# Kernel optimization log

Hardware: AMD Instinct MI355X
Metric: run time of the kernel (lower is better)

Reference implementation:

```python
import jax, jax.numpy as jnp
import numpy as np
from jax import lax

N = 25600      # total nodes = G * T
E = 204800     # edges (before self loops)
IN_CH = 6
HID = 64
HEADS = 4
G = 512        # graphs per batch
T = 50         # sequence length (node_time in [0, T))
OUT = 30       # prediction_horizon * 3
NEG_SLOPE = 0.2
BN_EPS = 1e-5


def _gat(x, src, dst, W, a_src, a_dst, b, heads, outc):
    # PyG GATConv (concat=True): h = x W reshaped to (N, H, C)
    n = x.shape[0]
    h = (x @ W).reshape(n, heads, outc)
    # edge scores: leaky_relu(a_src . h_src + a_dst . h_dst), softmax over incoming edges of dst
    e = jax.nn.leaky_relu((h * a_src).sum(-1)[src] + (h * a_dst).sum(-1)[dst], NEG_SLOPE)  # (E, H)
    m = jax.ops.segment_max(e, dst, num_segments=n)
    ex = jnp.exp(e - m[dst])
    denom = jax.ops.segment_sum(ex, dst, num_segments=n)
    alpha = ex / denom[dst]
    out = jax.ops.segment_sum(alpha[:, :, None] * h[src], dst, num_segments=n)  # (N, H, C)
    return out.reshape(n, heads * outc) + b


def _bn_eval(x, g, b):
    # BatchNorm in eval with running_mean=0, running_var=1
    return g * (x * (1.0 / np.float32(np.sqrt(1.0 + BN_EPS)))) + b


def setup_inputs() -> dict:
    ks = jax.random.split(jax.random.key(0), 16)
    s = 0.1
    d = {}
    d["x"] = jax.random.normal(ks[0], (N, IN_CH), jnp.float32)
    d["edge_index"] = jax.random.randint(ks[1], (2, E), 0, N)
    idx = jnp.arange(N)
    d["batch"] = idx // T       # each graph has exactly T nodes
    d["node_time"] = idx % T
    d["W1"] = jax.random.normal(ks[2], (IN_CH, HEADS * HID), jnp.float32) * s
    d["att_src1"] = jax.random.normal(ks[3], (HEADS, HID), jnp.float32) * s
    d["att_dst1"] = jax.random.normal(ks[4], (HEADS, HID), jnp.float32) * s
    d["b1"] = jnp.zeros((HEADS * HID,), jnp.float32)
    d["g1"] = jnp.ones((HEADS * HID,), jnp.float32)
    d["be1"] = jnp.zeros((HEADS * HID,), jnp.float32)
    d["W2"] = jax.random.normal(ks[5], (HEADS * HID, HID), jnp.float32) * s
    d["att_src2"] = jax.random.normal(ks[6], (1, HID), jnp.float32) * s
    d["att_dst2"] = jax.random.normal(ks[7], (1, HID), jnp.float32) * s
    d["b2"] = jnp.zeros((HID,), jnp.float32)
    d["g2"] = jnp.ones((HID,), jnp.float32)
    d["be2"] = jnp.zeros((HID,), jnp.float32)
    d["Wih"] = jax.random.normal(ks[8], (4 * HID, HID), jnp.float32) * s
    d["Whh"] = jax.random.normal(ks[9], (4 * HID, HID), jnp.float32) * s
    d["bih"] = jnp.zeros((4 * HID,), jnp.float32)
    d["bhh"] = jnp.zeros((4 * HID,), jnp.float32)
    d["Wfc"] = jax.random.normal(ks[10], (HID, OUT), jnp.float32) * s
    d["bfc"] = jnp.zeros((OUT,), jnp.float32)
    return d


def reference(x, edge_index, batch, node_time, W1, att_src1, att_dst1, b1, g1, be1,
              W2, att_src2, att_dst2, b2, g2, be2, Wih, Whh, bih, bhh, Wfc, bfc):
    loops = jnp.arange(N)
    src = jnp.concatenate([edge_index[0], loops])  # GATConv adds self loops
    dst = jnp.concatenate([edge_index[1], loops])
    h = jax.nn.elu(_bn_eval(_gat(x, src, dst, W1, att_src1, att_dst1, b1, HEADS, HID), g1, be1))
    h = jax.nn.elu(_bn_eval(_gat(h, src, dst, W2, att_src2, att_dst2, b2, 1, HID), g2, be2))
    # vectorized replacement of the per-node python scatter loop
    x_seq = jnp.zeros((G, T, HID), h.dtype).at[batch, node_time].set(h)

    def step(carry, xt):
        hh, cc = carry
        gates = xt @ Wih.T + bih + hh @ Whh.T + bhh
        i, f, gg, o = jnp.split(gates, 4, axis=-1)
        cc = jax.nn.sigmoid(f) * cc + jax.nn.sigmoid(i) * jnp.tanh(gg)
        hh = jax.nn.sigmoid(o) * jnp.tanh(cc)
        return (hh, cc), None

    init = (jnp.zeros((G, HID), h.dtype), jnp.zeros((G, HID), h.dtype))
    (hn, _), _ = lax.scan(step, init, x_seq.transpose(1, 0, 2))  # scan over time
    return hn @ Wfc + bfc  # (G, 30)
```

## Files before the change

### kernel.cpp

```cpp
#include <hip/hip_runtime.h>

#define N_NODES 25600
#define N_EDGES 204800
#define EE (N_EDGES + N_NODES)
#define IN_CH 6
#define HID 64
#define HEADS 4
#define G_GRAPHS 512
#define T_STEPS 50
#define OUT_DIM 30
#define NEG_SLOPE 0.2f
#define BN_INV 0.9999950000374997f

__device__ __forceinline__ float lrelu_(float x){ return x > 0.f ? x : NEG_SLOPE * x; }
__device__ __forceinline__ float elu_(float x){ return x > 0.f ? x : __expf(x) - 1.f; }
__device__ __forceinline__ float sigmoid_(float x){
    return __builtin_amdgcn_rcpf(1.f + __expf(-x));
}
__device__ __forceinline__ float tanh_(float x){
    return 1.f - 2.f * __builtin_amdgcn_rcpf(1.f + __expf(2.f * x));
}
__device__ __forceinline__ float bcast_(float v, int l){
    return __int_as_float(__builtin_amdgcn_readlane(__float_as_int(v), l));
}

__global__ void count_k(const int* __restrict__ ei, int* __restrict__ counts){
    int e = blockIdx.x * 256 + threadIdx.x;
    if (e >= EE) return;
    int dst = (e < N_EDGES) ? ei[N_EDGES + e] : (e - N_EDGES);
    atomicAdd(&counts[dst], 1);
}

__global__ void scan_k(const int* __restrict__ counts, int* __restrict__ row_ptr,
                       int* __restrict__ cursor){
    __shared__ int part[1024];
    int t = threadIdx.x;
    const int CH = N_NODES / 1024;
    int base = t * CH;
    int s = 0;
    for (int i = 0; i < CH; i++) s += counts[base + i];
    part[t] = s;
    __syncthreads();
    for (int off = 1; off < 1024; off <<= 1){
        int v = (t >= off) ? part[t - off] : 0;
        __syncthreads();
        part[t] += v;
        __syncthreads();
    }
    int run = (t > 0) ? part[t - 1] : 0;
    for (int i = 0; i < CH; i++){
        int cv = counts[base + i];
        row_ptr[base + i] = run;
        cursor[base + i]  = run;
        run += cv;
    }
    if (t == 1023) row_ptr[N_NODES] = run;
}

__global__ void scatter_k(const int* __restrict__ ei, int* __restrict__ cursor,
                          int* __restrict__ ssrc){
    int e = blockIdx.x * 256 + threadIdx.x;
    if (e >= EE) return;
    int src, dst;
    if (e < N_EDGES){ src = ei[e]; dst = ei[N_EDGES + e]; }
    else            { src = dst = e - N_EDGES; }
    int pos = atomicAdd(&cursor[dst], 1);
    ssrc[pos] = src;
}

__global__ void twih_k(const float* __restrict__ Wih, float* __restrict__ WihT){
    __shared__ float tile[64][65];
    int t = threadIdx.x;
    int jb = blockIdx.x * 64;
    for (int i = t; i < 64 * 64; i += 256){
        int j = i >> 6, k = i & 63;
        tile[k][j] = Wih[(size_t)(jb + j) * 64 + k];
    }
    __syncthreads();
    for (int i = t; i < 64 * 64; i += 256){
        int k = i >> 6, j = i & 63;
        WihT[(size_t)k * 256 + jb + j] = tile[k][j];
    }
}

__global__ void ns_k(const float* __restrict__ x, const float* __restrict__ W1,
                     const float* __restrict__ asw, const float* __restrict__ adw,
                     float* __restrict__ as1, float* __restrict__ ad1){
    __shared__ float waS[IN_CH * 4], waD[IN_CH * 4];
    int t = threadIdx.x;
    if (t < 48){
        int k = t >> 3, h = (t >> 1) & 3, which = t & 1;
        const float* a = which ? adw : asw;
        float s = 0.f;
        #pragma unroll
        for (int c = 0; c < 64; c++) s += W1[k * 256 + h * 64 + c] * a[h * 64 + c];
        (which ? waD : waS)[k * 4 + h] = s;
    }
    __syncthreads();
    int n = blockIdx.x * 256 + t;
    float xv[IN_CH];
    #pragma unroll
    for (int k = 0; k < IN_CH; k++) xv[k] = x[n * IN_CH + k];
    float sv[4] = {0.f, 0.f, 0.f, 0.f}, dv[4] = {0.f, 0.f, 0.f, 0.f};
    #pragma unroll
    for (int k = 0; k < IN_CH; k++){
        #pragma unroll
        for (int h = 0; h < 4; h++){
            sv[h] += xv[k] * waS[k * 4 + h];
            dv[h] += xv[k] * waD[k * 4 + h];
        }
    }
    *(float4*)&as1[n * 4] = make_float4(sv[0], sv[1], sv[2], sv[3]);
    *(float4*)&ad1[n * 4] = make_float4(dv[0], dv[1], dv[2], dv[3]);
}

__global__ void gat1_aggx(const float* __restrict__ x, const float* __restrict__ as1,
                          const float* __restrict__ ad1, const int* __restrict__ row_ptr,
                          const int* __restrict__ ssrc, const float* __restrict__ W1,
                          const float* __restrict__ b1, const float* __restrict__ g1,
                          const float* __restrict__ be1, float* __restrict__ h1_act){
    __shared__ float w1s[IN_CH * 256];
    int tid = threadIdx.x;
    for (int i = tid; i < IN_CH * 256; i += 256) w1s[i] = W1[i];
    __syncthreads();
    int wv = tid >> 6, lane = tid & 63;
    int n = blockIdx.x * 4 + wv;
    int s0 = row_ptr[n], s1 = row_ptr[n + 1];
    float4 adn = *(const float4*)&ad1[n * 4];
    float xs0[IN_CH] = {}, xs1[IN_CH] = {}, xs2[IN_CH] = {}, xs3[IN_CH] = {};
    float d0 = 0.f, d1 = 0.f, d2 = 0.f, d3 = 0.f;
    for (int j = s0; j < s1; j++){
        int s = ssrc[j];
        float4 as = *(const float4*)&as1[s * 4];
        float e0 = __expf(lrelu_(as.x + adn.x));
        float e1 = __expf(lrelu_(as.y + adn.y));
        float e2 = __expf(lrelu_(as.z + adn.z));
        float e3 = __expf(lrelu_(as.w + adn.w));
        d0 += e0; d1 += e1; d2 += e2; d3 += e3;
        const float2* xp = (const float2*)(x + (size_t)s * IN_CH);
        float2 xa = xp[0], xb = xp[1], xc = xp[2];
        float xv[IN_CH] = {xa.x, xa.y, xb.x, xb.y, xc.x, xc.y};
        #pragma unroll
        for (int k = 0; k < IN_CH; k++){
            xs0[k] += e0 * xv[k];
            xs1[k] += e1 * xv[k];
            xs2[k] += e2 * xv[k];
            xs3[k] += e3 * xv[k];
        }
    }
    float r0 = 1.f / d0, r1 = 1.f / d1, r2 = 1.f / d2, r3 = 1.f / d3;
    #pragma unroll
    for (int h = 0; h < 4; h++){
        const float* xsh = (h == 0) ? xs0 : (h == 1) ? xs1 : (h == 2) ? xs2 : xs3;
        float rh = (h == 0) ? r0 : (h == 1) ? r1 : (h == 2) ? r2 : r3;
        int col = h * 64 + lane;
        float acc = 0.f;
        #pragma unroll
        for (int k = 0; k < IN_CH; k++) acc += xsh[k] * w1s[k * 256 + col];
        float v = acc * rh + b1[col];
        v = g1[col] * (v * BN_INV) + be1[col];
        h1_act[(size_t)n * 256 + col] = elu_(v);
    }
}

#define TM 64
#define KT 32
#define APAD 4
__global__ __launch_bounds__(256) void gat2_tr(const float* __restrict__ h1_act,
                        const float* __restrict__ W2,
                        const float* __restrict__ asw, const float* __restrict__ adw,
                        float* __restrict__ h2_pre, float* __restrict__ as2,
                        float* __restrict__ ad2){
    __shared__ float As[TM][KT + APAD];
    __shared__ float Bs[KT][64];
    int tx = threadIdx.x;
    int rg = tx >> 4;
    int cg = tx & 15;
    int r0 = rg * 4, c0 = cg * 4;
    int rowBase = blockIdx.x * TM;
    float acc[4][4] = {};
    for (int k0 = 0; k0 < 256; k0 += KT){
        #pragma unroll
        for (int it = 0; it < 2; it++){
            int i = tx + it * 256;
            int row = i >> 3;
            int c4  = (i & 7) * 4;
            *(float4*)&As[row][c4] =
                *(const float4*)(h1_act + (size_t)(rowBase + row) * 256 + k0 + c4);
        }
        #pragma unroll
        for (int it = 0; it < 2; it++){
            int i = tx + it * 256;
            int row = i >> 4;
            int c4  = (i & 15) * 4;
            *(float4*)&Bs[row][c4] = *(const float4*)(W2 + (size_t)(k0 + row) * 64 + c4);
        }
        __syncthreads();
        #pragma unroll
        for (int kq = 0; kq < KT; kq += 4){
            float4 b0 = *(float4*)&Bs[kq + 0][c0];
            float4 b1v = *(float4*)&Bs[kq + 1][c0];
            float4 b2v = *(float4*)&Bs[kq + 2][c0];
            float4 b3 = *(float4*)&Bs[kq + 3][c0];
            #pragma unroll
            for (int i = 0; i < 4; i++){
                float4 a = *(float4*)&As[r0 + i][kq];
                acc[i][0] += a.x * b0.x + a.y * b1v.x + a.z * b2v.x + a.w * b3.x;
                acc[i][1] += a.x * b0.y + a.y * b1v.y + a.z * b2v.y + a.w * b3.y;
                acc[i][2] += a.x * b0.z + a.y * b1v.z + a.z * b2v.z + a.w * b3.z;
                acc[i][3] += a.x * b0.w + a.y * b1v.w + a.z * b2v.w + a.w * b3.w;
            }
        }
        __syncthreads();
    }
    float aw0 = asw[c0], aw1 = asw[c0+1], aw2 = asw[c0+2], aw3 = asw[c0+3];
    float dw0 = adw[c0], dw1 = adw[c0+1], dw2 = adw[c0+2], dw3 = adw[c0+3];
    #pragma unroll
    for (int i = 0; i < 4; i++){
        int row = rowBase + r0 + i;
        *(float4*)(h2_pre + (size_t)row * 64 + c0) =
            make_float4(acc[i][0], acc[i][1], acc[i][2], acc[i][3]);
        float sA = acc[i][0]*aw0 + acc[i][1]*aw1 + acc[i][2]*aw2 + acc[i][3]*aw3;
        float sD = acc[i][0]*dw0 + acc[i][1]*dw1 + acc[i][2]*dw2 + acc[i][3]*dw3;
        #pragma unroll
        for (int off = 8; off; off >>= 1){
            sA += __shfl_xor(sA, off);
            sD += __shfl_xor(sD, off);
        }
        if (cg == 0){ as2[row] = sA; ad2[row] = sD; }
    }
}

__global__ __launch_bounds__(256, 2) void gat2_aggp(const float* __restrict__ h2_pre,
        const float* __restrict__ as2, const float* __restrict__ ad2,
        const int* __restrict__ row_ptr, const int* __restrict__ ssrc,
        const float* __restrict__ b2, const float* __restrict__ g2,
        const float* __restrict__ be2,
        const int* __restrict__ batch, const int* __restrict__ ntime,
        const float* __restrict__ WihT, const float* __restrict__ bih,
        const float* __restrict__ bhh, float* __restrict__ gx){
    __shared__ float vsh[16][64];
    __shared__ int posb[16];
    int tx = threadIdx.x, wv = tx >> 6, lane = tx & 63;
    int nbase = blockIdx.x * 16;
    for (int q = 0; q < 4; q++){
        int n = nbase + wv * 4 + q;
        int s0 = row_ptr[n], s1 = row_ptr[n + 1];
        float adn = ad2[n];
        float denom = 0.f, acc = 0.f;
        int j = s0;
        for (; j + 4 <= s1; j += 4){
            int sa = ssrc[j], sb = ssrc[j + 1], sc = ssrc[j + 2], sd = ssrc[j + 3];
            float ea = __expf(lrelu_(as2[sa] + adn));
            float eb = __expf(lrelu_(as2[sb] + adn));
            float ec = __expf(lrelu_(as2[sc] + adn));
            float ed = __expf(lrelu_(as2[sd] + adn));
            float ha = h2_pre[(size_t)sa * 64 + lane];
            float hb = h2_pre[(size_t)sb * 64 + lane];
            float hc = h2_pre[(size_t)sc * 64 + lane];
            float hd = h2_pre[(size_t)sd * 64 + lane];
            denom += (ea + eb) + (ec + ed);
            acc += ea * ha + eb * hb + ec * hc + ed * hd;
        }
        for (; j < s1; j++){
            int s = ssrc[j];
            float e = __expf(lrelu_(as2[s] + adn));
            denom += e;
            acc += e * h2_pre[(size_t)s * 64 + lane];
        }
        float v = acc / denom + b2[lane];
        v = g2[lane] * (v * BN_INV) + be2[lane];
        vsh[wv * 4 + q][lane] = elu_(v);
        if (lane == 0) posb[wv * 4 + q] = batch[n] * T_STEPS + ntime[n];
    }
    __syncthreads();
    float vq[16];
    #pragma unroll
    for (int q = 0; q < 16; q++) vq[q] = vsh[q][lane];
    float bsum = bih[tx] + bhh[tx];
    float acc[16];
    #pragma unroll
    for (int q = 0; q < 16; q++) acc[q] = bsum;
    #pragma unroll 4
    for (int k = 0; k < 64; k++){
        float wk = WihT[(size_t)k * 256 + tx];
        #pragma unroll
        for (int q = 0; q < 16; q++)
            acc[q] += wk * bcast_(vq[q], k);
    }
    #pragma unroll
    for (int q = 0; q < 16; q++)
        gx[(size_t)posb[q] * 256 + tx] = acc[q];
}

__global__ __launch_bounds__(512, 2) void lstm_k(const float* __restrict__ gx,
        const float* __restrict__ Whh,
        const float* __restrict__ Wfc, const float* __restrict__ bfc,
        float* __restrict__ out){
    int g0 = blockIdx.x * 2;
    int t0 = threadIdx.x;
    int gr = t0 >> 8;
    int j  = t0 & 255;
    int lane = t0 & 63;
    __shared__ float gates[2][2][256];
    const float4* Wr = (const float4*)(Whh + (size_t)j * 64);
    const float* gxg = gx + (size_t)(g0 + gr) * T_STEPS * 256 + j;
    float c = 0.f, hn = 0.f;
    for (int t = 0; t < T_STEPS; t++){
        int buf = t & 1;
        float a0 = gxg[t * 256], a1 = 0.f, a2 = 0.f, a3 = 0.f;
        #pragma unroll
        for (int k = 0; k < 16; k++){
            float4 wv = Wr[k];
            a0 += wv.x * bcast_(hn, 4 * k + 0);
            a1 += wv.y * bcast_(hn, 4 * k + 1);
            a2 += wv.z * bcast_(hn, 4 * k + 2);
            a3 += wv.w * bcast_(hn, 4 * k + 3);
        }
        gates[gr][buf][j] = (a0 + a1) + (a2 + a3);
        __syncthreads();
        float iv = gates[gr][buf][lane];
        float fv = gates[gr][buf][64 + lane];
        float gv = gates[gr][buf][128 + lane];
        float ov = gates[gr][buf][192 + lane];
        c = sigmoid_(fv) * c + sigmoid_(iv) * tanh_(gv);
        hn = sigmoid_(ov) * tanh_(c);
    }
    if (j < 64) gates[gr][0][j] = hn;
    __syncthreads();
    if (j < OUT_DIM){
        float acc = bfc[j];
        #pragma unroll
        for (int k = 0; k < 64; k++) acc += gates[gr][0][k] * Wfc[k * OUT_DIM + j];
        out[(g0 + gr) * OUT_DIM + j] = acc;
    }
}

extern "C" void kernel_launch(void* const* d_in, const int* in_sizes, int n_in,
                              void* d_out, int out_size, void* d_ws, size_t ws_size,
                              hipStream_t stream){
    const float* x    = (const float*)d_in[0];
    const int*   ei   = (const int*)  d_in[1];
    const int*   batch= (const int*)  d_in[2];
    const int*   ntime= (const int*)  d_in[3];
    const float* W1   = (const float*)d_in[4];
    const float* as1w = (const float*)d_in[5];
    const float* ad1w = (const float*)d_in[6];
    const float* b1   = (const float*)d_in[7];
    const float* g1   = (const float*)d_in[8];
    const float* be1  = (const float*)d_in[9];
    const float* W2   = (const float*)d_in[10];
    const float* as2w = (const float*)d_in[11];
    const float* ad2w = (const float*)d_in[12];
    const float* b2   = (const float*)d_in[13];
    const float* g2   = (const float*)d_in[14];
    const float* be2  = (const float*)d_in[15];
    const float* Wih  = (const float*)d_in[16];
    const float* Whh  = (const float*)d_in[17];
    const float* bih  = (const float*)d_in[18];
    const float* bhh  = (const float*)d_in[19];
    const float* Wfc  = (const float*)d_in[20];
    const float* bfc  = (const float*)d_in[21];
    float* out = (float*)d_out;

    char* w = (char*)d_ws;
    auto alloc = [&](size_t bytes)->char*{
        char* p = w;
        w += (bytes + 255) & ~size_t(255);
        return p;
    };
    float* h1_act = (float*)alloc((size_t)N_NODES * 256 * 4);
    float* gx     = (float*)alloc((size_t)N_NODES * 256 * 4);
    float* h2_pre = (float*)alloc((size_t)N_NODES * 64 * 4);
    float* WihT   = (float*)alloc((size_t)64 * 256 * 4);
    float* as1    = (float*)alloc((size_t)N_NODES * 4 * 4);
    float* ad1    = (float*)alloc((size_t)N_NODES * 4 * 4);
    float* as2    = (float*)alloc((size_t)N_NODES * 4);
    float* ad2    = (float*)alloc((size_t)N_NODES * 4);
    int* counts   = (int*)alloc((size_t)N_NODES * 4);
    int* row_ptr  = (int*)alloc((size_t)(N_NODES + 1) * 4);
    int* cursor   = (int*)alloc((size_t)N_NODES * 4);
    int* ssrc     = (int*)alloc((size_t)EE * 4);

    hipMemsetAsync(counts, 0, (size_t)N_NODES * 4, stream);
    count_k  <<<(EE + 255) / 256, 256, 0, stream>>>(ei, counts);
    scan_k   <<<1, 1024, 0, stream>>>(counts, row_ptr, cursor);
    scatter_k<<<(EE + 255) / 256, 256, 0, stream>>>(ei, cursor, ssrc);
    twih_k   <<<4, 256, 0, stream>>>(Wih, WihT);
    ns_k     <<<N_NODES / 256, 256, 0, stream>>>(x, W1, as1w, ad1w, as1, ad1);
    gat1_aggx<<<N_NODES / 4, 256, 0, stream>>>(x, as1, ad1, row_ptr, ssrc, W1, b1, g1, be1, h1_act);
    gat2_tr  <<<N_NODES / TM, 256, 0, stream>>>(h1_act, W2, as2w, ad2w, h2_pre, as2, ad2);
    gat2_aggp<<<N_NODES / 16, 256, 0, stream>>>(h2_pre, as2, ad2, row_ptr, ssrc, b2, g2, be2,
                                                batch, ntime, WihT, bih, bhh, gx);
    lstm_k   <<<G_GRAPHS / 2, 512, 0, stream>>>(gx, Whh, Wfc, bfc, out);
}
```

Baseline: 296.6 us.

## Stage transposed Whh in LDS and process two graphs per thread in LSTM

The LSTM kernel now runs 256 threads per block, each handling one gate column for two graphs at once. It reads the recurrent weights from a transposed copy staged in shared memory (64 KB), instead of per-thread float4 loads from global memory. The input-gate values for the next timestep are prefetched, and a new transpose launch produces WhhT. The gat2 projection epilogue is also split into two passes of 8 accumulators to cut register pressure. The trade-offs are one extra small launch and heavy LDS use, which limits LSTM occupancy to very few blocks per CU.

Result: slower. 315.8 us (+6.5%).

```diff
diff --git a/kernel.cpp b/kernel.cpp
--- a/kernel.cpp
+++ b/kernel.cpp
@@ -68,18 +68,18 @@
     ssrc[pos] = src;
 }
 
-__global__ void twih_k(const float* __restrict__ Wih, float* __restrict__ WihT){
+__global__ void twih_k(const float* __restrict__ W, float* __restrict__ WT){
     __shared__ float tile[64][65];
     int t = threadIdx.x;
     int jb = blockIdx.x * 64;
     for (int i = t; i < 64 * 64; i += 256){
         int j = i >> 6, k = i & 63;
-        tile[k][j] = Wih[(size_t)(jb + j) * 64 + k];
+        tile[k][j] = W[(size_t)(jb + j) * 64 + k];
     }
     __syncthreads();
     for (int i = t; i < 64 * 64; i += 256){
         int k = i >> 6, j = i & 63;
-        WihT[(size_t)k * 256 + jb + j] = tile[k][j];
+        WT[(size_t)k * 256 + jb + j] = tile[k][j];
     }
 }
 
@@ -274,65 +274,102 @@
         if (lane == 0) posb[wv * 4 + q] = batch[n] * T_STEPS + ntime[n];
     }
     __syncthreads();
-    float vq[16];
-    #pragma unroll
-    for (int q = 0; q < 16; q++) vq[q] = vsh[q][lane];
     float bsum = bih[tx] + bhh[tx];
-    float acc[16];
-    #pragma unroll
-    for (int q = 0; q < 16; q++) acc[q] = bsum;
-    #pragma unroll 4
-    for (int k = 0; k < 64; k++){
-        float wk = WihT[(size_t)k * 256 + tx];
-        #pragma unroll
-        for (int q = 0; q < 16; q++)
-            acc[q] += wk * bcast_(vq[q], k);
-    }
-    #pragma unroll
-    for (int q = 0; q < 16; q++)
-        gx[(size_t)posb[q] * 256 + tx] = acc[q];
-}
-
-__global__ __launch_bounds__(512, 2) void lstm_k(const float* __restrict__ gx,
-        const float* __restrict__ Whh,
+    #pragma unroll 1
+    for (int pass = 0; pass < 2; pass++){
+        int qb = pass * 8;
+        float v0 = vsh[qb + 0][lane], v1 = vsh[qb + 1][lane];
+        float v2 = vsh[qb + 2][lane], v3 = vsh[qb + 3][lane];
+        float v4 = vsh[qb + 4][lane], v5 = vsh[qb + 5][lane];
+        float v6 = vsh[qb + 6][lane], v7 = vsh[qb + 7][lane];
+        float a0 = bsum, a1 = bsum, a2 = bsum, a3 = bsum;
+        float a4 = bsum, a5 = bsum, a6 = bsum, a7 = bsum;
+        #pragma unroll 8
+        for (int k = 0; k < 64; k++){
+            float wk = WihT[(size_t)k * 256 + tx];
+            a0 += wk * bcast_(v0, k);
+            a1 += wk * bcast_(v1, k);
+            a2 += wk * bcast_(v2, k);
+            a3 += wk * bcast_(v3, k);
+            a4 += wk * bcast_(v4, k);
+            a5 += wk * bcast_(v5, k);
+            a6 += wk * bcast_(v6, k);
+            a7 += wk * bcast_(v7, k);
+        }
+        gx[(size_t)posb[qb + 0] * 256 + tx] = a0;
+        gx[(size_t)posb[qb + 1] * 256 + tx] = a1;
+        gx[(size_t)posb[qb + 2] * 256 + tx] = a2;
+        gx[(size_t)posb[qb + 3] * 256 + tx] = a3;
+        gx[(size_t)posb[qb + 4] * 256 + tx] = a4;
+        gx[(size_t)posb[qb + 5] * 256 + tx] = a5;
+        gx[(size_t)posb[qb + 6] * 256 + tx] = a6;
+        gx[(size_t)posb[qb + 7] * 256 + tx] = a7;
+    }
+}
+
+__global__ __launch_bounds__(256) void lstm_k(const float* __restrict__ gx,
+        const float* __restrict__ WhhT,
         const float* __restrict__ Wfc, const float* __restrict__ bfc,
         float* __restrict__ out){
+    __shared__ float wsh[64 * 256];
+    __shared__ float gates[2][2][256];
     int g0 = blockIdx.x * 2;
-    int t0 = threadIdx.x;
-    int gr = t0 >> 8;
-    int j  = t0 & 255;
-    int lane = t0 & 63;
-    __shared__ float gates[2][2][256];
-    const float4* Wr = (const float4*)(Whh + (size_t)j * 64);
-    const float* gxg = gx + (size_t)(g0 + gr) * T_STEPS * 256 + j;
-    float c = 0.f, hn = 0.f;
+    int tx = threadIdx.x;
+    int lane = tx & 63;
+    const float4* Wg = (const float4*)WhhT;
+    float4* Ws = (float4*)wsh;
+    #pragma unroll
+    for (int i = 0; i < 16; i++) Ws[tx + i * 256] = Wg[tx + i * 256];
+    __syncthreads();
+    const float* gxA = gx + (size_t)g0 * T_STEPS * 256;
+    const float* gxB = gx + (size_t)(g0 + 1) * T_STEPS * 256;
+    float ga = gxA[tx], gb = gxB[tx];
+    float cA = 0.f, hA = 0.f, cB = 0.f, hB = 0.f;
     for (int t = 0; t < T_STEPS; t++){
+        float na = 0.f, nb = 0.f;
+        if (t + 1 < T_STEPS){
+            na = gxA[(t + 1) * 256 + tx];
+            nb = gxB[(t + 1) * 256 + tx];
+        }
+        float a = ga, b = gb;
+        #pragma unroll
+        for (int k = 0; k < 64; k++){
+            float wk = wsh[k * 256 + tx];
+            a += wk * bcast_(hA, k);
+            b += wk * bcast_(hB, k);
+        }
         int buf = t & 1;
-        float a0 = gxg[t * 256], a1 = 0.f, a2 = 0.f, a3 = 0.f;
-        #pragma unroll
-        for (int k = 0; k < 16; k++){
-            float4 wv = Wr[k];
-            a0 += wv.x * bcast_(hn, 4 * k + 0);
-            a1 += wv.y * bcast_(hn, 4 * k + 1);
-            a2 += wv.z * bcast_(hn, 4 * k + 2);
-            a3 += wv.w * bcast_(hn, 4 * k + 3);
-        }
-        gates[gr][buf][j] = (a0 + a1) + (a2 + a3);
+        gates[0][buf][tx] = a;
+        gates[1][buf][tx] = b;
         __syncthreads();
-        float iv = gates[gr][buf][lane];
-        float fv = gates[gr][buf][64 + lane];
-        float gv = gates[gr][buf][128 + lane];
-        float ov = gates[gr][buf][192 + lane];
-        c = sigmoid_(fv) * c + sigmoid_(iv) * tanh_(gv);
-        hn = sigmoid_(ov) * tanh_(c);
-    }
-    if (j < 64) gates[gr][0][j] = hn;
-    __syncthreads();
-    if (j < OUT_DIM){
+        float iA = gates[0][buf][lane];
+        float fA = gates[0][buf][64 + lane];
+        float gA = gates[0][buf][128 + lane];
+        float oA = gates[0][buf][192 + lane];
+        float iB = gates[1][buf][lane];
+        float fB = gates[1][buf][64 + lane];
+        float gB = gates[1][buf][128 + lane];
+        float oB = gates[1][buf][192 + lane];
+        cA = sigmoid_(fA) * cA + sigmoid_(iA) * tanh_(gA);
+        hA = sigmoid_(oA) * tanh_(cA);
+        cB = sigmoid_(fB) * cB + sigmoid_(iB) * tanh_(gB);
+        hB = sigmoid_(oB) * tanh_(cB);
+        ga = na; gb = nb;
+    }
+    if (tx < 64) gates[0][0][tx] = hA;
+    else if (tx >= 128 && tx < 192) gates[1][0][tx - 128] = hB;
+    __syncthreads();
+    if (tx < OUT_DIM){
+        float acc = bfc[tx];
+        #pragma unroll
+        for (int k = 0; k < 64; k++) acc += gates[0][0][k] * Wfc[k * OUT_DIM + tx];
+        out[g0 * OUT_DIM + tx] = acc;
+    } else if (tx >= 128 && tx < 128 + OUT_DIM){
+        int j = tx - 128;
         float acc = bfc[j];
         #pragma unroll
-        for (int k = 0; k < 64; k++) acc += gates[gr][0][k] * Wfc[k * OUT_DIM + j];
-        out[(g0 + gr) * OUT_DIM + j] = acc;
+        for (int k = 0; k < 64; k++) acc += gates[1][0][k] * Wfc[k * OUT_DIM + j];
+        out[(g0 + 1) * OUT_DIM + j] = acc;
     }
 }
 
@@ -373,6 +410,7 @@
     float* gx     = (float*)alloc((size_t)N_NODES * 256 * 4);
     float* h2_pre = (float*)alloc((size_t)N_NODES * 64 * 4);
     float* WihT   = (float*)alloc((size_t)64 * 256 * 4);
+    float* WhhT   = (float*)alloc((size_t)64 * 256 * 4);
     float* as1    = (float*)alloc((size_t)N_NODES * 4 * 4);
     float* ad1    = (float*)alloc((size_t)N_NODES * 4 * 4);
     float* as2    = (float*)alloc((size_t)N_NODES * 4);
@@ -387,10 +425,11 @@
     scan_k   <<<1, 1024, 0, stream>>>(counts, row_ptr, cursor);
     scatter_k<<<(EE + 255) / 256, 256, 0, stream>>>(ei, cursor, ssrc);
     twih_k   <<<4, 256, 0, stream>>>(Wih, WihT);
+    twih_k   <<<4, 256, 0, stream>>>(Whh, WhhT);
     ns_k     <<<N_NODES / 256, 256, 0, stream>>>(x, W1, as1w, ad1w, as1, ad1);
     gat1_aggx<<<N_NODES / 4, 256, 0, stream>>>(x, as1, ad1, row_ptr, ssrc, W1, b1, g1, be1, h1_act);
     gat2_tr  <<<N_NODES / TM, 256, 0, stream>>>(h1_act, W2, as2w, ad2w, h2_pre, as2, ad2);
     gat2_aggp<<<N_NODES / 16, 256, 0, stream>>>(h2_pre, as2, ad2, row_ptr, ssrc, b2, g2, be2,
                                                 batch, ntime, WihT, bih, bhh, gx);
-    lstm_k   <<<G_GRAPHS / 2, 512, 0, stream>>>(gx, Whh, Wfc, bfc, out);
-}
+    lstm_k   <<<G_GRAPHS / 2, 256, 0, stream>>>(gx, WhhT, Wfc, bfc, out);
+}
```
